# Kernel tuning notes

Hardware: AMD Instinct MI355X
Metric: run time of the kernel (lower is better)

Reference implementation:

```python
import jax, jax.numpy as jnp
import numpy as np

H = 128  # GRU hidden size


def gru_cell(x_t, h, W_ih, W_hh, b_ih, b_hh):
    # Standard torch GRU cell math.
    gi = x_t @ W_ih.T + b_ih            # (bs, 3H)
    gh = h @ W_hh.T + b_hh              # (bs, 3H)
    i_r, i_z, i_n = jnp.split(gi, 3, axis=-1)
    h_r, h_z, h_n = jnp.split(gh, 3, axis=-1)
    r = jax.nn.sigmoid(i_r + h_r)
    z = jax.nn.sigmoid(i_z + h_z)
    n = jnp.tanh(i_n + r * h_n)
    return (1.0 - z) * n + z * h


def setup_inputs() -> dict:
    key = jax.random.key(0)
    ks = jax.random.split(key, 16)
    bs, seq, emb, nc = 64, 1024, 300, 23
    s = 0.05
    inp = {
        "x": jax.random.normal(ks[0], (bs, seq, emb), jnp.float32),
        "adj": jax.random.uniform(ks[1], (bs, seq, seq), jnp.float32),
        "mask": jax.random.uniform(ks[2], (bs, seq, 1), jnp.float32),
        # GRU forward direction params (torch layout: W_ih (3H, emb), W_hh (3H, H))
        "W_ih_f": jax.random.normal(ks[3], (3 * H, emb), jnp.float32) * s,
        "W_hh_f": jax.random.normal(ks[4], (3 * H, H), jnp.float32) * s,
        "b_ih_f": jax.random.normal(ks[5], (3 * H,), jnp.float32) * s,
        "b_hh_f": jax.random.normal(ks[6], (3 * H,), jnp.float32) * s,
        # GRU backward direction params
        "W_ih_b": jax.random.normal(ks[7], (3 * H, emb), jnp.float32) * s,
        "W_hh_b": jax.random.normal(ks[8], (3 * H, H), jnp.float32) * s,
        "b_ih_b": jax.random.normal(ks[9], (3 * H,), jnp.float32) * s,
        "b_hh_b": jax.random.normal(ks[10], (3 * H,), jnp.float32) * s,
        # MLP head: Linear(300+256,128) -> Linear(128,64) -> Linear(64,23)
        "W1": jax.random.normal(ks[11], (128, emb + 2 * H), jnp.float32) * s,
        "b1": jnp.zeros((128,), jnp.float32),
        "W2": jax.random.normal(ks[12], (64, 128), jnp.float32) * s,
        "b2": jnp.zeros((64,), jnp.float32),
        "W3": jax.random.normal(ks[13], (nc, 64), jnp.float32) * s,
        "b3": jnp.zeros((nc,), jnp.float32),
    }
    return inp


def reference(x, adj, mask, W_ih_f, W_hh_f, b_ih_f, b_hh_f,
              W_ih_b, W_hh_b, b_ih_b, b_hh_b, W1, b1, W2, b2, W3, b3):
    x = x * mask                                   # (bs, seq, emb)
    bs, seq, emb = x.shape

    # --- bidirectional GRU, last-step output ---
    # Forward direction output at t = seq-1 is the final hidden of a full scan.
    h0 = jnp.zeros((bs, H), x.dtype)
    def step(h, x_t):
        h_new = gru_cell(x_t, h, W_ih_f, W_hh_f, b_ih_f, b_hh_f)
        return h_new, None
    h_fwd, _ = jax.lax.scan(step, h0, jnp.swapaxes(x, 0, 1))  # (bs, H)
    # Backward direction output at t = seq-1 is exactly ONE cell step on x[:, -1]
    # starting from the zero initial state (it has only consumed the last token).
    h_bwd = gru_cell(x[:, -1, :], h0, W_ih_b, W_hh_b, b_ih_b, b_hh_b)
    h = jnp.concatenate([h_fwd, h_bwd], axis=1)    # (bs, 2H)

    # --- gfm: sum_{i,j} x_i * x_j per feature == (sum_i x_i)^2 ---
    # (original code materializes a (bs, seq*seq, emb) tensor; adj is dead code)
    s = jnp.sum(x, axis=1)                         # (bs, emb)
    gfm = s * s                                    # (bs, emb)

    # --- MLP head (dropout is identity at eval) ---
    z = jnp.concatenate([h, gfm], axis=1)          # (bs, 2H + emb)
    z = jax.nn.relu(z @ W1.T + b1)
    z = jax.nn.relu(z @ W2.T + b2)
    logit = z @ W3.T + b3                          # (bs, num_class)
    return logit
```

## Files before the change

### kernel.cpp

```cpp
#include <hip/hip_runtime.h>
#include <hip/hip_bf16.h>

#define HH   128
#define EMB  300
#define SEQ  1024
#define BS   64
#define NG   384
#define NCHUNK 8

typedef __attribute__((ext_vector_type(8))) short  bf16x8;
typedef __attribute__((ext_vector_type(4))) float  f32x4;
typedef _Float16 f16x2 __attribute__((ext_vector_type(2)));

__device__ __forceinline__ unsigned short f2bf(float f) {
    unsigned int u = __float_as_uint(f);
    unsigned int r = (u + 0x7fffu + ((u >> 16) & 1u)) >> 16;
    return (unsigned short)r;
}
__device__ __forceinline__ float fexp(float x) { return __builtin_amdgcn_exp2f(x * 1.44269504088896f); }
__device__ __forceinline__ float fsig(float x) { return __builtin_amdgcn_rcpf(1.f + fexp(-x)); }
__device__ __forceinline__ float ftanh(float x){ return __builtin_amdgcn_rcpf(1.f + fexp(-2.f*x)) * 2.f - 1.f; }

__device__ __forceinline__ float dpp_pair_add(float x) {
    int y = __builtin_amdgcn_mov_dpp(__float_as_int(x), 0xB1, 0xF, 0xF, true);
    return x + __int_as_float(y);
}

#define BAR_LDS() asm volatile("s_waitcnt lgkmcnt(0)\n\ts_barrier" ::: "memory")

__global__ __launch_bounds__(256) void gi_gemm(const float* __restrict__ X,
                                               const float* __restrict__ mask,
                                               const float* __restrict__ W,
                                               const float* __restrict__ bias,
                                               float* __restrict__ out) {
    __shared__ __align__(16) unsigned short As[128 * 32];
    __shared__ __align__(16) unsigned short Bs[128 * 32];
    const int m0   = blockIdx.x * 128;
    const int n0   = blockIdx.y * 128;
    const int tid  = threadIdx.x;
    const int row  = tid >> 1;
    const int seg  = tid & 1;
    const int wave = tid >> 6;
    const int lane = tid & 63;
    const int wr   = wave >> 1, wc = wave & 1;
    const int r16  = lane & 15, kg = lane >> 4;

    f32x4 acc[4][4];
    #pragma unroll
    for (int m = 0; m < 4; ++m)
        #pragma unroll
        for (int n = 0; n < 4; ++n) acc[m][n] = (f32x4){0.f,0.f,0.f,0.f};

    const float mrow = mask[m0 + row];

    for (int k0 = 0; k0 < 320; k0 += 32) {
        {
            const float* src = X + (size_t)(m0 + row) * EMB + k0 + seg * 16;
            unsigned short tmp[16];
            if (k0 + seg * 16 + 15 < EMB) {
                #pragma unroll
                for (int i = 0; i < 4; ++i) {
                    float4 v = ((const float4*)src)[i];
                    tmp[i*4+0] = f2bf(v.x * mrow);
                    tmp[i*4+1] = f2bf(v.y * mrow);
                    tmp[i*4+2] = f2bf(v.z * mrow);
                    tmp[i*4+3] = f2bf(v.w * mrow);
                }
            } else {
                #pragma unroll
                for (int i = 0; i < 16; ++i) {
                    int c = k0 + seg * 16 + i;
                    float v = (c < EMB) ? src[i] : 0.f;
                    tmp[i] = f2bf(v * mrow);
                }
            }
            uint4* dst = (uint4*)&As[row * 32 + seg * 16];
            dst[0] = ((const uint4*)tmp)[0];
            dst[1] = ((const uint4*)tmp)[1];
        }
        {
            const float* src = W + (size_t)(n0 + row) * EMB + k0 + seg * 16;
            unsigned short tmp[16];
            if (k0 + seg * 16 + 15 < EMB) {
                #pragma unroll
                for (int i = 0; i < 4; ++i) {
                    float4 v = ((const float4*)src)[i];
                    tmp[i*4+0] = f2bf(v.x);
                    tmp[i*4+1] = f2bf(v.y);
                    tmp[i*4+2] = f2bf(v.z);
                    tmp[i*4+3] = f2bf(v.w);
                }
            } else {
                #pragma unroll
                for (int i = 0; i < 16; ++i) {
                    int c = k0 + seg * 16 + i;
                    float v = (c < EMB) ? src[i] : 0.f;
                    tmp[i] = f2bf(v);
                }
            }
            uint4* dst = (uint4*)&Bs[row * 32 + seg * 16];
            dst[0] = ((const uint4*)tmp)[0];
            dst[1] = ((const uint4*)tmp)[1];
        }
        __syncthreads();

        bf16x8 a[4], bfr[4];
        #pragma unroll
        for (int m = 0; m < 4; ++m)
            a[m] = *(const bf16x8*)&As[(wr * 64 + m * 16 + r16) * 32 + kg * 8];
        #pragma unroll
        for (int n = 0; n < 4; ++n)
            bfr[n] = *(const bf16x8*)&Bs[(wc * 64 + n * 16 + r16) * 32 + kg * 8];
        #pragma unroll
        for (int m = 0; m < 4; ++m)
            #pragma unroll
            for (int n = 0; n < 4; ++n)
                acc[m][n] = __builtin_amdgcn_mfma_f32_16x16x32_bf16(a[m], bfr[n], acc[m][n], 0, 0, 0);
        __syncthreads();
    }

    #pragma unroll
    for (int m = 0; m < 4; ++m) {
        const int rowb = m0 + wr * 64 + m * 16 + (lane >> 4) * 4;
        #pragma unroll
        for (int n = 0; n < 4; ++n) {
            const int col = n0 + wc * 64 + n * 16 + r16;
            const float bj = bias[col];
            #pragma unroll
            for (int q = 0; q < 4; ++q)
                out[(size_t)(rowb + q) * NG + col] = acc[m][n][q] + bj;
        }
    }
}

__global__ __launch_bounds__(320) void col_sum(const float* __restrict__ X,
                                               const float* __restrict__ mask,
                                               float* __restrict__ spart) {
    const int b = blockIdx.x, c = blockIdx.y;
    const int e = threadIdx.x;
    if (e >= EMB) return;
    const int tchunk = SEQ / NCHUNK;
    float acc = 0.f;
    const float* xb = X + ((size_t)b * SEQ + (size_t)c * tchunk) * EMB;
    const float* mb = mask + (size_t)b * SEQ + (size_t)c * tchunk;
    for (int t = 0; t < tchunk; ++t)
        acc += xb[(size_t)t * EMB + e] * mb[t];
    spart[((size_t)b * NCHUNK + c) * EMB + e] = acc;
}

__global__ __launch_bounds__(256, 1) void gru_scan(const float* __restrict__ gi,
                                                   const float* __restrict__ Whh,
                                                   const float* __restrict__ bhh,
                                                   float* __restrict__ hout) {
    const int b    = blockIdx.x;
    const int tid  = threadIdx.x;
    const int j    = tid >> 1;
    const int half = tid & 1;
    __shared__ __align__(16) _Float16 hb[2][HH];

    f16x2 wr_[32], wz_[32], wn_[32];
    {
        const float2* r0 = (const float2*)(Whh + (size_t)j * HH            + half * 64);
        const float2* r1 = (const float2*)(Whh + (size_t)(j + HH) * HH     + half * 64);
        const float2* r2 = (const float2*)(Whh + (size_t)(j + 2 * HH) * HH + half * 64);
        #pragma unroll
        for (int i = 0; i < 32; ++i) {
            float2 a = r0[i], c = r1[i], d = r2[i];
            wr_[i] = (f16x2){(_Float16)a.x, (_Float16)a.y};
            wz_[i] = (f16x2){(_Float16)c.x, (_Float16)c.y};
            wn_[i] = (f16x2){(_Float16)d.x, (_Float16)d.y};
        }
    }
    const float br_ = bhh[j], bz_ = bhh[j + HH], bn_ = bhh[j + 2 * HH];

    float hreg = 0.f;
    if (tid < HH) hb[0][tid] = (_Float16)0.f;
    const float* gb = gi + (size_t)b * SEQ * NG;

    float gAr, gAz, gAn, gBr, gBz, gBn, gCr, gCz, gCn, gDr, gDz, gDn;
    {
        const float* g0 = gb;               gAr = g0[j]; gAz = g0[j+HH]; gAn = g0[j+2*HH];
        const float* g1 = gb + NG;          gBr = g1[j]; gBz = g1[j+HH]; gBn = g1[j+2*HH];
        const float* g2 = gb + 2 * NG;      gCr = g2[j]; gCz = g2[j+HH]; gCn = g2[j+2*HH];
        const float* g3 = gb + 3 * NG;      gDr = g3[j]; gDz = g3[j+HH]; gDn = g3[j+2*HH];
    }
    const float* pA = gb + 4 * NG;
    const float* pB = gb + 5 * NG;
    const float* pC = gb + 6 * NG;
    const float* pD = gb + 7 * NG;
    BAR_LDS();

#define GRU_BODY(P, GR, GZ, GN, PP)                                            \
    {                                                                          \
        float ar[2] = {0.f, 0.f}, az[2] = {0.f, 0.f}, an[2] = {0.f, 0.f};      \
        const uint4* hp = (const uint4*)&hb[P][half * 64];                     \
        _Pragma("unroll")                                                      \
        for (int i = 0; i < 8; ++i) {                                          \
            union { uint4 u; f16x2 h2[4]; } U;                                 \
            U.u = hp[i];                                                       \
            _Pragma("unroll")                                                  \
            for (int k = 0; k < 4; ++k) {                                      \
                ar[k&1] = __builtin_amdgcn_fdot2(wr_[i*4+k], U.h2[k], ar[k&1], false); \
                az[k&1] = __builtin_amdgcn_fdot2(wz_[i*4+k], U.h2[k], az[k&1], false); \
                an[k&1] = __builtin_amdgcn_fdot2(wn_[i*4+k], U.h2[k], an[k&1], false); \
            }                                                                  \
        }                                                                      \
        const float arf = dpp_pair_add(ar[0] + ar[1]);                         \
        const float azf = dpp_pair_add(az[0] + az[1]);                         \
        const float anf = dpp_pair_add(an[0] + an[1]);                         \
        const float r = fsig(GR + arf + br_);                                  \
        const float z = fsig(GZ + azf + bz_);                                  \
        const float n = ftanh(GN + r * (anf + bn_));                           \
        hreg = n + z * (hreg - n);                                             \
        hb[P ^ 1][j] = (_Float16)hreg;                                         \
        GR = PP[j]; GZ = PP[j + HH]; GN = PP[j + 2 * HH];                      \
        PP += 4 * NG;                                                          \
        BAR_LDS();                                                             \
    }

    for (int it = 0; it < SEQ / 4; ++it) {
        GRU_BODY(0, gAr, gAz, gAn, pA)
        GRU_BODY(1, gBr, gBz, gBn, pB)
        GRU_BODY(0, gCr, gCz, gCn, pC)
        GRU_BODY(1, gDr, gDz, gDn, pD)
    }
#undef GRU_BODY
    if (!half) hout[b * HH + j] = hreg;
}

__global__ __launch_bounds__(384) void gru_bwd(const float* __restrict__ X,
                                               const float* __restrict__ mask,
                                               const float* __restrict__ Wih,
                                               const float* __restrict__ bih,
                                               const float* __restrict__ bhh,
                                               float* __restrict__ hout) {
    const int b = blockIdx.x, j = threadIdx.x;
    __shared__ float gib[NG];
    const float* xr = X + ((size_t)b * SEQ + (SEQ - 1)) * EMB;
    const float  mv = mask[(size_t)b * SEQ + SEQ - 1];
    const float* wr_ = Wih + (size_t)j * EMB;
    float acc = 0.f;
    for (int e = 0; e < EMB; ++e) acc += xr[e] * wr_[e];
    gib[j] = acc * mv + bih[j];
    __syncthreads();
    if (j < HH) {
        const float r = fsig(gib[j] + bhh[j]);
        const float z = fsig(gib[j + HH] + bhh[j + HH]);
        const float n = ftanh(gib[j + 2 * HH] + r * bhh[j + 2 * HH]);
        hout[b * HH + j] = (1.f - z) * n;
    }
}

__global__ __launch_bounds__(128) void mlp(const float* __restrict__ hf,
                                           const float* __restrict__ hb,
                                           const float* __restrict__ spart,
                                           const float* __restrict__ W1, const float* __restrict__ b1,
                                           const float* __restrict__ W2, const float* __restrict__ b2,
                                           const float* __restrict__ W3, const float* __restrict__ b3,
                                           float* __restrict__ out) {
    const int b = blockIdx.x, j = threadIdx.x;
    __shared__ float zin[2 * HH + EMB];
    __shared__ float l1[128];
    __shared__ float l2[64];
    zin[j]      = hf[b * HH + j];
    zin[HH + j] = hb[b * HH + j];
    for (int e = j; e < EMB; e += 128) {
        float v = 0.f;
        #pragma unroll
        for (int c = 0; c < NCHUNK; ++c)
            v += spart[((size_t)b * NCHUNK + c) * EMB + e];
        zin[2 * HH + e] = v * v;
    }
    __syncthreads();
    {
        float a = b1[j];
        const float* w = W1 + (size_t)j * (2 * HH + EMB);
        for (int i = 0; i < 2 * HH + EMB; ++i) a += zin[i] * w[i];
        l1[j] = fmaxf(a, 0.f);
    }
    __syncthreads();
    if (j < 64) {
        float a = b2[j];
        const float* w = W2 + (size_t)j * 128;
        for (int i = 0; i < 128; ++i) a += l1[i] * w[i];
        l2[j] = fmaxf(a, 0.f);
    }
    __syncthreads();
    if (j < 23) {
        float a = b3[j];
        const float* w = W3 + (size_t)j * 64;
        for (int i = 0; i < 64; ++i) a += l2[i] * w[i];
        out[b * 23 + j] = a;
    }
}

extern "C" void kernel_launch(void* const* d_in, const int* in_sizes, int n_in,
                              void* d_out, int out_size, void* d_ws, size_t ws_size,
                              hipStream_t stream) {
    const float* x     = (const float*)d_in[0];
    const float* mask  = (const float*)d_in[2];
    const float* Wih_f = (const float*)d_in[3];
    const float* Whh_f = (const float*)d_in[4];
    const float* bih_f = (const float*)d_in[5];
    const float* bhh_f = (const float*)d_in[6];
    const float* Wih_b = (const float*)d_in[7];
    const float* bih_b = (const float*)d_in[9];
    const float* bhh_b = (const float*)d_in[10];
    const float* W1 = (const float*)d_in[11];
    const float* b1 = (const float*)d_in[12];
    const float* W2 = (const float*)d_in[13];
    const float* b2 = (const float*)d_in[14];
    const float* W3 = (const float*)d_in[15];
    const float* b3 = (const float*)d_in[16];
    float* out = (float*)d_out;

    float* gi    = (float*)d_ws;
    float* spart = gi + (size_t)BS * SEQ * NG;
    float* hf    = spart + (size_t)BS * NCHUNK * EMB;
    float* hb    = hf + BS * HH;

    gi_gemm<<<dim3(512, 3), dim3(256), 0, stream>>>(x, mask, Wih_f, bih_f, gi);
    col_sum<<<dim3(BS, NCHUNK), dim3(320), 0, stream>>>(x, mask, spart);
    gru_scan<<<dim3(BS), dim3(256), 0, stream>>>(gi, Whh_f, bhh_f, hf);
    gru_bwd<<<dim3(BS), dim3(384), 0, stream>>>(x, mask, Wih_b, bih_b, bhh_b, hb);
    mlp<<<dim3(BS), dim3(128), 0, stream>>>(hf, hb, spart, W1, b1, W2, b2, W3, b3, out);
}
```

Baseline: 527.1 us.

## Store gate preactivations as bf16, fold biases, widen GEMM tile, fuse backward cell into MLP

The input-gate GEMM now writes its output as bf16 instead of fp32, halving the gi buffer that the sequential GRU scan reads every step. It also folds the r/z hidden biases into that output. The GEMM is retiled to one block covering all 384 columns with 512 threads, so each X tile is loaded and converted once instead of three times. The backward one-step GRU cell is merged into the MLP kernel to remove a launch, and only one of each thread pair writes h to LDS. The cost is reduced precision of the gate preactivations, which risks accuracy drift over the 1024-step recurrence.

```diff
diff --git a/kernel.cpp b/kernel.cpp
--- a/kernel.cpp
+++ b/kernel.cpp
@@ -17,6 +17,9 @@
     unsigned int r = (u + 0x7fffu + ((u >> 16) & 1u)) >> 16;
     return (unsigned short)r;
 }
+__device__ __forceinline__ float bf2f(unsigned short u) {
+    return __uint_as_float((unsigned int)u << 16);
+}
 __device__ __forceinline__ float fexp(float x) { return __builtin_amdgcn_exp2f(x * 1.44269504088896f); }
 __device__ __forceinline__ float fsig(float x) { return __builtin_amdgcn_rcpf(1.f + fexp(-x)); }
 __device__ __forceinline__ float ftanh(float x){ return __builtin_amdgcn_rcpf(1.f + fexp(-2.f*x)) * 2.f - 1.f; }
@@ -28,107 +31,100 @@
 
 #define BAR_LDS() asm volatile("s_waitcnt lgkmcnt(0)\n\ts_barrier" ::: "memory")
 
-__global__ __launch_bounds__(256) void gi_gemm(const float* __restrict__ X,
+__global__ __launch_bounds__(512) void gi_gemm(const float* __restrict__ X,
                                                const float* __restrict__ mask,
                                                const float* __restrict__ W,
                                                const float* __restrict__ bias,
-                                               float* __restrict__ out) {
+                                               const float* __restrict__ bhh2,
+                                               unsigned short* __restrict__ out) {
     __shared__ __align__(16) unsigned short As[128 * 32];
-    __shared__ __align__(16) unsigned short Bs[128 * 32];
+    __shared__ __align__(16) unsigned short Bs[384 * 32];
     const int m0   = blockIdx.x * 128;
-    const int n0   = blockIdx.y * 128;
     const int tid  = threadIdx.x;
-    const int row  = tid >> 1;
-    const int seg  = tid & 1;
+    const int row  = tid >> 2;
+    const int seg  = tid & 3;
     const int wave = tid >> 6;
     const int lane = tid & 63;
-    const int wr   = wave >> 1, wc = wave & 1;
+    const int wm   = wave >> 2;
+    const int wn   = wave & 3;
     const int r16  = lane & 15, kg = lane >> 4;
 
-    f32x4 acc[4][4];
+    f32x4 acc[4][6];
     #pragma unroll
     for (int m = 0; m < 4; ++m)
         #pragma unroll
-        for (int n = 0; n < 4; ++n) acc[m][n] = (f32x4){0.f,0.f,0.f,0.f};
+        for (int n = 0; n < 6; ++n) acc[m][n] = (f32x4){0.f,0.f,0.f,0.f};
 
     const float mrow = mask[m0 + row];
 
     for (int k0 = 0; k0 < 320; k0 += 32) {
         {
-            const float* src = X + (size_t)(m0 + row) * EMB + k0 + seg * 16;
-            unsigned short tmp[16];
-            if (k0 + seg * 16 + 15 < EMB) {
-                #pragma unroll
-                for (int i = 0; i < 4; ++i) {
-                    float4 v = ((const float4*)src)[i];
-                    tmp[i*4+0] = f2bf(v.x * mrow);
-                    tmp[i*4+1] = f2bf(v.y * mrow);
-                    tmp[i*4+2] = f2bf(v.z * mrow);
-                    tmp[i*4+3] = f2bf(v.w * mrow);
-                }
+            const float* src = X + (size_t)(m0 + row) * EMB + k0 + seg * 8;
+            unsigned short tmp[8];
+            if (k0 + seg * 8 + 7 < EMB) {
+                float4 v0 = ((const float4*)src)[0];
+                float4 v1 = ((const float4*)src)[1];
+                tmp[0]=f2bf(v0.x*mrow); tmp[1]=f2bf(v0.y*mrow);
+                tmp[2]=f2bf(v0.z*mrow); tmp[3]=f2bf(v0.w*mrow);
+                tmp[4]=f2bf(v1.x*mrow); tmp[5]=f2bf(v1.y*mrow);
+                tmp[6]=f2bf(v1.z*mrow); tmp[7]=f2bf(v1.w*mrow);
             } else {
                 #pragma unroll
-                for (int i = 0; i < 16; ++i) {
-                    int c = k0 + seg * 16 + i;
+                for (int i = 0; i < 8; ++i) {
+                    int c = k0 + seg * 8 + i;
                     float v = (c < EMB) ? src[i] : 0.f;
                     tmp[i] = f2bf(v * mrow);
                 }
             }
-            uint4* dst = (uint4*)&As[row * 32 + seg * 16];
-            dst[0] = ((const uint4*)tmp)[0];
-            dst[1] = ((const uint4*)tmp)[1];
-        }
-        {
-            const float* src = W + (size_t)(n0 + row) * EMB + k0 + seg * 16;
-            unsigned short tmp[16];
-            if (k0 + seg * 16 + 15 < EMB) {
-                #pragma unroll
-                for (int i = 0; i < 4; ++i) {
-                    float4 v = ((const float4*)src)[i];
-                    tmp[i*4+0] = f2bf(v.x);
-                    tmp[i*4+1] = f2bf(v.y);
-                    tmp[i*4+2] = f2bf(v.z);
-                    tmp[i*4+3] = f2bf(v.w);
-                }
+            *(uint4*)&As[row * 32 + seg * 8] = *(const uint4*)tmp;
+        }
+        #pragma unroll
+        for (int r3 = 0; r3 < 3; ++r3) {
+            const int rowb = row + r3 * 128;
+            const float* src = W + (size_t)rowb * EMB + k0 + seg * 8;
+            unsigned short tmp[8];
+            if (k0 + seg * 8 + 7 < EMB) {
+                float4 v0 = ((const float4*)src)[0];
+                float4 v1 = ((const float4*)src)[1];
+                tmp[0]=f2bf(v0.x); tmp[1]=f2bf(v0.y); tmp[2]=f2bf(v0.z); tmp[3]=f2bf(v0.w);
+                tmp[4]=f2bf(v1.x); tmp[5]=f2bf(v1.y); tmp[6]=f2bf(v1.z); tmp[7]=f2bf(v1.w);
             } else {
                 #pragma unroll
-                for (int i = 0; i < 16; ++i) {
-                    int c = k0 + seg * 16 + i;
+                for (int i = 0; i < 8; ++i) {
+                    int c = k0 + seg * 8 + i;
                     float v = (c < EMB) ? src[i] : 0.f;
                     tmp[i] = f2bf(v);
                 }
             }
-            uint4* dst = (uint4*)&Bs[row * 32 + seg * 16];
-            dst[0] = ((const uint4*)tmp)[0];
-            dst[1] = ((const uint4*)tmp)[1];
+            *(uint4*)&Bs[rowb * 32 + seg * 8] = *(const uint4*)tmp;
         }
         __syncthreads();
 
-        bf16x8 a[4], bfr[4];
+        bf16x8 a[4], bfr[6];
         #pragma unroll
         for (int m = 0; m < 4; ++m)
-            a[m] = *(const bf16x8*)&As[(wr * 64 + m * 16 + r16) * 32 + kg * 8];
-        #pragma unroll
-        for (int n = 0; n < 4; ++n)
-            bfr[n] = *(const bf16x8*)&Bs[(wc * 64 + n * 16 + r16) * 32 + kg * 8];
+            a[m] = *(const bf16x8*)&As[(wm * 64 + m * 16 + r16) * 32 + kg * 8];
+        #pragma unroll
+        for (int n = 0; n < 6; ++n)
+            bfr[n] = *(const bf16x8*)&Bs[(wn * 96 + n * 16 + r16) * 32 + kg * 8];
         #pragma unroll
         for (int m = 0; m < 4; ++m)
             #pragma unroll
-            for (int n = 0; n < 4; ++n)
+            for (int n = 0; n < 6; ++n)
                 acc[m][n] = __builtin_amdgcn_mfma_f32_16x16x32_bf16(a[m], bfr[n], acc[m][n], 0, 0, 0);
         __syncthreads();
     }
 
     #pragma unroll
     for (int m = 0; m < 4; ++m) {
-        const int rowb = m0 + wr * 64 + m * 16 + (lane >> 4) * 4;
-        #pragma unroll
-        for (int n = 0; n < 4; ++n) {
-            const int col = n0 + wc * 64 + n * 16 + r16;
-            const float bj = bias[col];
+        const int rowb = m0 + wm * 64 + m * 16 + kg * 4;
+        #pragma unroll
+        for (int n = 0; n < 6; ++n) {
+            const int col = wn * 96 + n * 16 + r16;
+            const float bj = bias[col] + (col < 2 * HH ? bhh2[col] : 0.f);
             #pragma unroll
             for (int q = 0; q < 4; ++q)
-                out[(size_t)(rowb + q) * NG + col] = acc[m][n][q] + bj;
+                out[(size_t)(rowb + q) * NG + col] = f2bf(acc[m][n][q] + bj);
         }
     }
 }
@@ -148,7 +144,7 @@
     spart[((size_t)b * NCHUNK + c) * EMB + e] = acc;
 }
 
-__global__ __launch_bounds__(256, 1) void gru_scan(const float* __restrict__ gi,
+__global__ __launch_bounds__(256, 1) void gru_scan(const unsigned short* __restrict__ gi,
                                                    const float* __restrict__ Whh,
                                                    const float* __restrict__ bhh,
                                                    float* __restrict__ hout) {
@@ -171,23 +167,23 @@
             wn_[i] = (f16x2){(_Float16)d.x, (_Float16)d.y};
         }
     }
-    const float br_ = bhh[j], bz_ = bhh[j + HH], bn_ = bhh[j + 2 * HH];
+    const float bn_ = bhh[j + 2 * HH];
 
     float hreg = 0.f;
     if (tid < HH) hb[0][tid] = (_Float16)0.f;
-    const float* gb = gi + (size_t)b * SEQ * NG;
+    const unsigned short* gb = gi + (size_t)b * SEQ * NG;
 
     float gAr, gAz, gAn, gBr, gBz, gBn, gCr, gCz, gCn, gDr, gDz, gDn;
     {
-        const float* g0 = gb;               gAr = g0[j]; gAz = g0[j+HH]; gAn = g0[j+2*HH];
-        const float* g1 = gb + NG;          gBr = g1[j]; gBz = g1[j+HH]; gBn = g1[j+2*HH];
-        const float* g2 = gb + 2 * NG;      gCr = g2[j]; gCz = g2[j+HH]; gCn = g2[j+2*HH];
-        const float* g3 = gb + 3 * NG;      gDr = g3[j]; gDz = g3[j+HH]; gDn = g3[j+2*HH];
-    }
-    const float* pA = gb + 4 * NG;
-    const float* pB = gb + 5 * NG;
-    const float* pC = gb + 6 * NG;
-    const float* pD = gb + 7 * NG;
+        const unsigned short* g0 = gb;          gAr = bf2f(g0[j]); gAz = bf2f(g0[j+HH]); gAn = bf2f(g0[j+2*HH]);
+        const unsigned short* g1 = gb + NG;     gBr = bf2f(g1[j]); gBz = bf2f(g1[j+HH]); gBn = bf2f(g1[j+2*HH]);
+        const unsigned short* g2 = gb + 2 * NG; gCr = bf2f(g2[j]); gCz = bf2f(g2[j+HH]); gCn = bf2f(g2[j+2*HH]);
+        const unsigned short* g3 = gb + 3 * NG; gDr = bf2f(g3[j]); gDz = bf2f(g3[j+HH]); gDn = bf2f(g3[j+2*HH]);
+    }
+    const unsigned short* pA = gb + 4 * NG;
+    const unsigned short* pB = gb + 5 * NG;
+    const unsigned short* pC = gb + 6 * NG;
+    const unsigned short* pD = gb + 7 * NG;
     BAR_LDS();
 
 #define GRU_BODY(P, GR, GZ, GN, PP)                                            \
@@ -208,12 +204,12 @@
         const float arf = dpp_pair_add(ar[0] + ar[1]);                         \
         const float azf = dpp_pair_add(az[0] + az[1]);                         \
         const float anf = dpp_pair_add(an[0] + an[1]);                         \
-        const float r = fsig(GR + arf + br_);                                  \
-        const float z = fsig(GZ + azf + bz_);                                  \
+        const float r = fsig(GR + arf);                                        \
+        const float z = fsig(GZ + azf);                                        \
         const float n = ftanh(GN + r * (anf + bn_));                           \
         hreg = n + z * (hreg - n);                                             \
-        hb[P ^ 1][j] = (_Float16)hreg;                                         \
-        GR = PP[j]; GZ = PP[j + HH]; GN = PP[j + 2 * HH];                      \
+        if (!half) hb[P ^ 1][j] = (_Float16)hreg;                              \
+        GR = bf2f(PP[j]); GZ = bf2f(PP[j + HH]); GN = bf2f(PP[j + 2 * HH]);    \
         PP += 4 * NG;                                                          \
         BAR_LDS();                                                             \
     }
@@ -228,42 +224,27 @@
     if (!half) hout[b * HH + j] = hreg;
 }
 
-__global__ __launch_bounds__(384) void gru_bwd(const float* __restrict__ X,
-                                               const float* __restrict__ mask,
-                                               const float* __restrict__ Wih,
-                                               const float* __restrict__ bih,
-                                               const float* __restrict__ bhh,
-                                               float* __restrict__ hout) {
-    const int b = blockIdx.x, j = threadIdx.x;
-    __shared__ float gib[NG];
-    const float* xr = X + ((size_t)b * SEQ + (SEQ - 1)) * EMB;
-    const float  mv = mask[(size_t)b * SEQ + SEQ - 1];
-    const float* wr_ = Wih + (size_t)j * EMB;
-    float acc = 0.f;
-    for (int e = 0; e < EMB; ++e) acc += xr[e] * wr_[e];
-    gib[j] = acc * mv + bih[j];
-    __syncthreads();
-    if (j < HH) {
-        const float r = fsig(gib[j] + bhh[j]);
-        const float z = fsig(gib[j + HH] + bhh[j + HH]);
-        const float n = ftanh(gib[j + 2 * HH] + r * bhh[j + 2 * HH]);
-        hout[b * HH + j] = (1.f - z) * n;
-    }
-}
-
-__global__ __launch_bounds__(128) void mlp(const float* __restrict__ hf,
-                                           const float* __restrict__ hb,
+__global__ __launch_bounds__(128) void mlp(const float* __restrict__ X,
+                                           const float* __restrict__ mask,
+                                           const float* __restrict__ WihB,
+                                           const float* __restrict__ bihB,
+                                           const float* __restrict__ bhhB,
+                                           const float* __restrict__ hf,
                                            const float* __restrict__ spart,
                                            const float* __restrict__ W1, const float* __restrict__ b1,
                                            const float* __restrict__ W2, const float* __restrict__ b2,
                                            const float* __restrict__ W3, const float* __restrict__ b3,
                                            float* __restrict__ out) {
     const int b = blockIdx.x, j = threadIdx.x;
+    __shared__ float xl[EMB];
     __shared__ float zin[2 * HH + EMB];
     __shared__ float l1[128];
     __shared__ float l2[64];
-    zin[j]      = hf[b * HH + j];
-    zin[HH + j] = hb[b * HH + j];
+
+    const float* xr = X + ((size_t)b * SEQ + (SEQ - 1)) * EMB;
+    const float  mv = mask[(size_t)b * SEQ + SEQ - 1];
+    for (int e = j; e < EMB; e += 128) xl[e] = xr[e];
+    zin[j] = hf[b * HH + j];
     for (int e = j; e < EMB; e += 128) {
         float v = 0.f;
         #pragma unroll
@@ -272,6 +253,23 @@
         zin[2 * HH + e] = v * v;
     }
     __syncthreads();
+
+    {
+        const float* wR = WihB + (size_t)j * EMB;
+        const float* wZ = WihB + (size_t)(j + HH) * EMB;
+        const float* wN = WihB + (size_t)(j + 2 * HH) * EMB;
+        float aR = 0.f, aZ = 0.f, aN = 0.f;
+        for (int e = 0; e < EMB; ++e) {
+            const float xv = xl[e];
+            aR += xv * wR[e]; aZ += xv * wZ[e]; aN += xv * wN[e];
+        }
+        const float r = fsig(aR * mv + bihB[j] + bhhB[j]);
+        const float z = fsig(aZ * mv + bihB[j + HH] + bhhB[j + HH]);
+        const float n = ftanh(aN * mv + bihB[j + 2 * HH] + r * bhhB[j + 2 * HH]);
+        zin[HH + j] = (1.f - z) * n;
+    }
+    __syncthreads();
+
     {
         float a = b1[j];
         const float* w = W1 + (size_t)j * (2 * HH + EMB);
@@ -314,14 +312,13 @@
     const float* b3 = (const float*)d_in[16];
     float* out = (float*)d_out;
 
-    float* gi    = (float*)d_ws;
-    float* spart = gi + (size_t)BS * SEQ * NG;
+    unsigned short* gi16 = (unsigned short*)d_ws;
+    float* spart = (float*)(gi16 + (size_t)BS * SEQ * NG);
     float* hf    = spart + (size_t)BS * NCHUNK * EMB;
-    float* hb    = hf + BS * HH;
-
-    gi_gemm<<<dim3(512, 3), dim3(256), 0, stream>>>(x, mask, Wih_f, bih_f, gi);
+
+    gi_gemm<<<dim3(512), dim3(512), 0, stream>>>(x, mask, Wih_f, bih_f, bhh_f, gi16);
     col_sum<<<dim3(BS, NCHUNK), dim3(320), 0, stream>>>(x, mask, spart);
-    gru_scan<<<dim3(BS), dim3(256), 0, stream>>>(gi, Whh_f, bhh_f, hf);
-    gru_bwd<<<dim3(BS), dim3(384), 0, stream>>>(x, mask, Wih_b, bih_b, bhh_b, hb);
-    mlp<<<dim3(BS), dim3(128), 0, stream>>>(hf, hb, spart, W1, b1, W2, b2, W3, b3, out);
-}
+    gru_scan<<<dim3(BS), dim3(256), 0, stream>>>(gi16, Whh_f, bhh_f, hf);
+    mlp<<<dim3(BS), dim3(128), 0, stream>>>(x, mask, Wih_b, bih_b, bhh_b, hf, spart,
+                                            W1, b1, W2, b2, W3, b3, out);
+}
```

Result: slower. 579.0 us (+9.9%).
